# Kernel optimization log

Hardware: AMD Instinct MI355X
Metric: run time of the kernel (lower is better)

The kernel has to match this reference:

```python
import jax, jax.numpy as jnp
import numpy as np

D_MODEL = 768
NHEAD = 12
HEAD_DIM = D_MODEL // NHEAD


def setup_inputs() -> dict:
    key = jax.random.key(0)
    ks = jax.random.split(key, 9)
    B, S = 1, 4096
    scale = 1.0 / np.sqrt(D_MODEL)
    x = jax.random.normal(ks[0], (B, S, D_MODEL), dtype=jnp.float32)
    # Linear params: weight [out,in] torch convention, bias [out]
    wq = jax.random.normal(ks[1], (D_MODEL, D_MODEL), dtype=jnp.float32) * scale
    bq = jnp.zeros((D_MODEL,), dtype=jnp.float32)
    wk = jax.random.normal(ks[2], (D_MODEL, D_MODEL), dtype=jnp.float32) * scale
    bk = jnp.zeros((D_MODEL,), dtype=jnp.float32)
    wv = jax.random.normal(ks[3], (D_MODEL, D_MODEL), dtype=jnp.float32) * scale
    bv = jnp.zeros((D_MODEL,), dtype=jnp.float32)
    wo = jax.random.normal(ks[4], (D_MODEL, D_MODEL), dtype=jnp.float32) * scale
    bo = jnp.zeros((D_MODEL,), dtype=jnp.float32)
    return {"x": x, "wq": wq, "bq": bq, "wk": wk, "bk": bk,
            "wv": wv, "bv": bv, "wo": wo, "bo": bo}


def reference(x, wq, bq, wk, bk, wv, bv, wo, bo):
    B, S, D = x.shape
    H, Hd = NHEAD, HEAD_DIM
    # projections (torch Linear: x @ W^T + b)
    q = (x @ wq.T + bq).reshape(B, S, H, Hd).transpose(0, 2, 1, 3)  # [B,H,S,Hd]
    k = (x @ wk.T + bk).reshape(B, S, H, Hd).transpose(0, 2, 1, 3)
    v = (x @ wv.T + bv).reshape(B, S, H, Hd).transpose(0, 2, 1, 3)
    scores = jnp.einsum('bhsd,bhtd->bhst', q, k) / jnp.sqrt(jnp.float32(Hd))  # [B,H,S,S]
    probs = jax.nn.softmax(scores, axis=-1)
    attn = jnp.einsum('bhst,bhtd->bhsd', probs, v)  # [B,H,S,Hd]
    attn = attn.transpose(0, 2, 1, 3).reshape(B, S, D)
    return attn @ wo.T + bo
```

## Files before the change

### kernel.cpp

```cpp
#include <hip/hip_runtime.h>
#include <hip/hip_bf16.h>

typedef __attribute__((ext_vector_type(8))) __bf16 bf16x8;
typedef __attribute__((ext_vector_type(4))) __bf16 bf16x4;
typedef __attribute__((ext_vector_type(4))) float f32x4;

#define D_MODEL 768
#define SEQ     4096
#define NH      12
#define HD      64

#define QSCALE (0.125f * 1.44269504088896f)

__device__ __forceinline__ void gload_lds16(const void* g, void* l) {
    __builtin_amdgcn_global_load_lds(
        (const __attribute__((address_space(1))) void*)g,
        (__attribute__((address_space(3))) void*)l, 16, 0, 0);
}

__global__ __launch_bounds__(256) void cvt_kernel(
    const float* __restrict__ x,  const float* __restrict__ wq,
    const float* __restrict__ wk, const float* __restrict__ wv,
    const float* __restrict__ wo,
    __bf16* __restrict__ xb,  __bf16* __restrict__ wqb,
    __bf16* __restrict__ wkb, __bf16* __restrict__ wvb,
    __bf16* __restrict__ wob)
{
    const int XV = SEQ * D_MODEL / 4;
    const int WV = D_MODEL * D_MODEL / 4;
    const int total = XV + 4 * WV;
    for (int i = blockIdx.x * blockDim.x + threadIdx.x; i < total;
         i += gridDim.x * blockDim.x) {
        const float* src; __bf16* dst; int j;
        if      (i < XV)          { src = x;  dst = xb;  j = i; }
        else if (i < XV + WV)     { src = wq; dst = wqb; j = i - XV; }
        else if (i < XV + 2*WV)   { src = wk; dst = wkb; j = i - XV - WV; }
        else if (i < XV + 3*WV)   { src = wv; dst = wvb; j = i - XV - 2*WV; }
        else                      { src = wo; dst = wob; j = i - XV - 3*WV; }
        float4 v = ((const float4*)src)[j];
        bf16x4 o;
        o[0] = (__bf16)v.x; o[1] = (__bf16)v.y;
        o[2] = (__bf16)v.z; o[3] = (__bf16)v.w;
        ((bf16x4*)dst)[j] = o;
    }
}

__device__ __forceinline__ void gemm128_core(
    const __bf16* __restrict__ A, const __bf16* __restrict__ B, int KD,
    f32x4 acc[4][4], __bf16 (*As)[64], __bf16 (*Bs)[64])
{
    const int t = threadIdx.x;
    const int lane = t & 63, wid = t >> 6;
    const int wm = (wid & 1) * 64, wn = (wid >> 1) * 64;
    const int lr = lane & 15, lc = lane >> 4;
    const int rl = lane >> 3;
    const int cs = (lane & 7) ^ rl;

    const __bf16* ag = A + (size_t)(wid * 32 + rl) * KD + cs * 8;
    const __bf16* bg = B + (size_t)(wid * 32 + rl) * KD + cs * 8;

    for (int kt = 0; kt < KD / 64; ++kt) {
        __syncthreads();
        #pragma unroll
        for (int i = 0; i < 4; ++i) {
            gload_lds16(ag + (size_t)i * 8 * KD + kt * 64,
                        &As[wid * 32 + i * 8][0]);
            gload_lds16(bg + (size_t)i * 8 * KD + kt * 64,
                        &Bs[wid * 32 + i * 8][0]);
        }
        __syncthreads();

        #pragma unroll
        for (int kh = 0; kh < 2; ++kh) {
            bf16x8 af[4], bfr[4];
            #pragma unroll
            for (int mi = 0; mi < 4; ++mi)
                af[mi] = *(const bf16x8*)
                    &As[wm + mi * 16 + lr][(((kh << 2) | lc) ^ (lr & 7)) * 8];
            #pragma unroll
            for (int ni = 0; ni < 4; ++ni)
                bfr[ni] = *(const bf16x8*)
                    &Bs[wn + ni * 16 + lr][(((kh << 2) | lc) ^ (lr & 7)) * 8];
            __builtin_amdgcn_s_setprio(1);
            #pragma unroll
            for (int mi = 0; mi < 4; ++mi)
                #pragma unroll
                for (int ni = 0; ni < 4; ++ni)
                    acc[mi][ni] = __builtin_amdgcn_mfma_f32_16x16x32_bf16(
                        af[mi], bfr[ni], acc[mi][ni], 0, 0, 0);
            __builtin_amdgcn_s_setprio(0);
        }
    }
}

__global__ __launch_bounds__(256) void qkv_gemm(
    const __bf16* __restrict__ xb,
    const __bf16* __restrict__ wqb, const __bf16* __restrict__ wkb,
    const __bf16* __restrict__ wvb,
    const float* __restrict__ bq, const float* __restrict__ bk,
    const float* __restrict__ bv,
    __bf16* __restrict__ Qo, __bf16* __restrict__ Ko,
    __bf16* __restrict__ Vto)
{
    __shared__ __bf16 As[128][64];
    __shared__ __bf16 Bs[128][64];
    const int bm = blockIdx.x;
    const int seg = blockIdx.y / 6, bn = blockIdx.y % 6;
    const __bf16* B  = (seg == 0) ? wqb : (seg == 1) ? wkb : wvb;
    const float* bias = (seg == 0) ? bq : (seg == 1) ? bk : bv;

    f32x4 acc[4][4] = {};
    gemm128_core(xb + (size_t)bm * 128 * D_MODEL,
                 B  + (size_t)bn * 128 * D_MODEL, D_MODEL, acc, As, Bs);

    const int t = threadIdx.x, lane = t & 63, wid = t >> 6;
    const int wm = (wid & 1) * 64, wn = (wid >> 1) * 64;
    const int lr = lane & 15, lc = lane >> 4;
    const int m0 = bm * 128 + wm, n0 = bn * 128 + wn;

    if (seg < 2) {
        __bf16* O = (seg == 0) ? Qo : Ko;
        const float sc = (seg == 0) ? QSCALE : 1.0f;
        #pragma unroll
        for (int mi = 0; mi < 4; ++mi)
            #pragma unroll
            for (int ni = 0; ni < 4; ++ni) {
                int col = n0 + ni * 16 + lr;
                float bb = bias[col];
                #pragma unroll
                for (int r = 0; r < 4; ++r)
                    O[(size_t)(m0 + mi * 16 + lc * 4 + r) * D_MODEL + col] =
                        (__bf16)((acc[mi][ni][r] + bb) * sc);
            }
    } else {
        #pragma unroll
        for (int mi = 0; mi < 4; ++mi)
            #pragma unroll
            for (int ni = 0; ni < 4; ++ni) {
                int col = n0 + ni * 16 + lr;
                float bb = bias[col];
                bf16x4 pk;
                #pragma unroll
                for (int r = 0; r < 4; ++r)
                    pk[r] = (__bf16)(acc[mi][ni][r] + bb);
                *(bf16x4*)&Vto[(size_t)col * SEQ + m0 + mi * 16 + lc * 4] = pk;
            }
    }
}

__global__ __launch_bounds__(256) void attn_kernel(
    const __bf16* __restrict__ Q, const __bf16* __restrict__ K,
    const __bf16* __restrict__ Vt, __bf16* __restrict__ Attn)
{
    __shared__ __bf16 Ks[2][64][64];
    __shared__ __bf16 Vs[2][64][64];
    __shared__ __bf16 Ps[4][16][64];

    const int bid = blockIdx.x;
    const int swz = (bid & 7) * 96 + (bid >> 3);
    const int h  = swz >> 6;
    const int q0 = (swz & 63) * 64;

    const int t = threadIdx.x, lane = t & 63, wid = t >> 6;
    const int lr = lane & 15, lc = lane >> 4;
    const int rl = lane >> 3;
    const int cs = (lane & 7) ^ rl;
    const int sx = lr & 7;

    const __bf16* kg = K  + (size_t)(wid * 16 + rl) * D_MODEL + h * HD + cs * 8;
    const __bf16* vg = Vt + (size_t)(h * HD + wid * 16 + rl) * SEQ + cs * 8;

    const __bf16* qrow = Q + (size_t)(q0 + wid * 16 + lr) * D_MODEL + h * HD;
    bf16x8 qf0 = *(const bf16x8*)&qrow[lc * 8];
    bf16x8 qf1 = *(const bf16x8*)&qrow[32 + lc * 8];

    f32x4 acc[4] = {};
    float m_r = -1e30f, l_r = 0.f;

    {
        gload_lds16(kg,                 &Ks[0][wid * 16 + 0][0]);
        gload_lds16(kg + 8 * D_MODEL,   &Ks[0][wid * 16 + 8][0]);
        gload_lds16(vg,                 &Vs[0][wid * 16 + 0][0]);
        gload_lds16(vg + 8 * SEQ,       &Vs[0][wid * 16 + 8][0]);
    }

    const int NT = SEQ / 64;
    for (int kt = 0; kt < NT; ++kt) {
        const int cur = kt & 1;
        __syncthreads();

        if (kt + 1 < NT) {
            const int nxt = cur ^ 1;
            const size_t ko = (size_t)(kt + 1) * 64 * D_MODEL;
            const size_t vo = (size_t)(kt + 1) * 64;
            gload_lds16(kg + ko,               &Ks[nxt][wid * 16 + 0][0]);
            gload_lds16(kg + ko + 8 * D_MODEL, &Ks[nxt][wid * 16 + 8][0]);
            gload_lds16(vg + vo,               &Vs[nxt][wid * 16 + 0][0]);
            gload_lds16(vg + vo + 8 * SEQ,     &Vs[nxt][wid * 16 + 8][0]);
        }

        bf16x8 kf[4][2];
        #pragma unroll
        for (int nt = 0; nt < 4; ++nt) {
            kf[nt][0] = *(const bf16x8*)&Ks[cur][nt * 16 + lr][(lc ^ sx) * 8];
            kf[nt][1] = *(const bf16x8*)&Ks[cur][nt * 16 + lr][((4 | lc) ^ sx) * 8];
        }
        f32x4 st[4];
        __builtin_amdgcn_s_setprio(1);
        #pragma unroll
        for (int nt = 0; nt < 4; ++nt) {
            f32x4 s = {};
            s = __builtin_amdgcn_mfma_f32_16x16x32_bf16(kf[nt][0], qf0, s, 0, 0, 0);
            s = __builtin_amdgcn_mfma_f32_16x16x32_bf16(kf[nt][1], qf1, s, 0, 0, 0);
            st[nt] = s;
        }
        __builtin_amdgcn_s_setprio(0);

        float mx = -1e30f;
        #pragma unroll
        for (int nt = 0; nt < 4; ++nt)
            #pragma unroll
            for (int r = 0; r < 4; ++r)
                mx = fmaxf(mx, st[nt][r]);
        mx = fmaxf(mx, __shfl_xor(mx, 16, 64));
        mx = fmaxf(mx, __shfl_xor(mx, 32, 64));

        const bool skip = (bool)__all(mx - m_r <= 8.0f);
        float mnew = skip ? m_r : fmaxf(m_r, mx);
        float corr = skip ? 1.0f : exp2f(m_r - mnew);

        float rs = 0.f;
        float pv[4][4];
        #pragma unroll
        for (int nt = 0; nt < 4; ++nt)
            #pragma unroll
            for (int r = 0; r < 4; ++r) {
                float p = exp2f(st[nt][r] - mnew);
                pv[nt][r] = p;
                rs += p;
            }
        rs += __shfl_xor(rs, 16, 64);
        rs += __shfl_xor(rs, 32, 64);
        l_r = l_r * corr + rs;
        m_r = mnew;

        if (!skip) {
            #pragma unroll
            for (int r = 0; r < 4; ++r) {
                float cq = __shfl(corr, lc * 4 + r, 64);
                #pragma unroll
                for (int dt = 0; dt < 4; ++dt)
                    acc[dt][r] *= cq;
            }
        }

        #pragma unroll
        for (int nt = 0; nt < 4; ++nt) {
            union { __bf16 hh[4]; uint2 u; } w;
            w.hh[0] = (__bf16)pv[nt][0]; w.hh[1] = (__bf16)pv[nt][1];
            w.hh[2] = (__bf16)pv[nt][2]; w.hh[3] = (__bf16)pv[nt][3];
            const int pb = (((nt << 1) | (lc >> 1)) ^ sx) * 8 + (lc & 1) * 4;
            *(uint2*)&Ps[wid][lr][pb] = w.u;
        }

        bf16x8 pa0 = *(const bf16x8*)&Ps[wid][lr][(lc ^ sx) * 8];
        bf16x8 pa1 = *(const bf16x8*)&Ps[wid][lr][((4 | lc) ^ sx) * 8];
        __builtin_amdgcn_s_setprio(1);
        #pragma unroll
        for (int dt = 0; dt < 4; ++dt) {
            bf16x8 vf0 = *(const bf16x8*)&Vs[cur][dt * 16 + lr][(lc ^ sx) * 8];
            bf16x8 vf1 = *(const bf16x8*)&Vs[cur][dt * 16 + lr][((4 | lc) ^ sx) * 8];
            acc[dt] = __builtin_amdgcn_mfma_f32_16x16x32_bf16(pa0, vf0, acc[dt], 0, 0, 0);
            acc[dt] = __builtin_amdgcn_mfma_f32_16x16x32_bf16(pa1, vf1, acc[dt], 0, 0, 0);
        }
        __builtin_amdgcn_s_setprio(0);
    }

    #pragma unroll
    for (int r = 0; r < 4; ++r) {
        float linv = 1.0f / __shfl(l_r, lc * 4 + r, 64);
        #pragma unroll
        for (int dt = 0; dt < 4; ++dt)
            Attn[(size_t)(q0 + wid * 16 + lc * 4 + r) * D_MODEL
                 + h * HD + dt * 16 + lr] = (__bf16)(acc[dt][r] * linv);
    }
}

__global__ __launch_bounds__(256) void out_gemm(
    const __bf16* __restrict__ Ab, const __bf16* __restrict__ wob,
    const float* __restrict__ bo, float* __restrict__ out)
{
    __shared__ __bf16 As[128][64];
    __shared__ __bf16 Bs[128][64];
    const int bm = blockIdx.x, bn = blockIdx.y;
    f32x4 acc[4][4] = {};
    gemm128_core(Ab  + (size_t)bm * 128 * D_MODEL,
                 wob + (size_t)bn * 128 * D_MODEL, D_MODEL, acc, As, Bs);

    const int t = threadIdx.x, lane = t & 63, wid = t >> 6;
    const int wm = (wid & 1) * 64, wn = (wid >> 1) * 64;
    const int lr = lane & 15, lc = lane >> 4;
    const int m0 = bm * 128 + wm, n0 = bn * 128 + wn;
    #pragma unroll
    for (int mi = 0; mi < 4; ++mi)
        #pragma unroll
        for (int ni = 0; ni < 4; ++ni) {
            int col = n0 + ni * 16 + lr;
            float bb = bo[col];
            #pragma unroll
            for (int r = 0; r < 4; ++r)
                out[(size_t)(m0 + mi * 16 + lc * 4 + r) * D_MODEL + col] =
                    acc[mi][ni][r] + bb;
        }
}

extern "C" void kernel_launch(void* const* d_in, const int* in_sizes, int n_in,
                              void* d_out, int out_size, void* d_ws, size_t ws_size,
                              hipStream_t stream) {
    const float* x  = (const float*)d_in[0];
    const float* wq = (const float*)d_in[1];
    const float* bq = (const float*)d_in[2];
    const float* wk = (const float*)d_in[3];
    const float* bk = (const float*)d_in[4];
    const float* wv = (const float*)d_in[5];
    const float* bv = (const float*)d_in[6];
    const float* wo = (const float*)d_in[7];
    const float* bo = (const float*)d_in[8];

    char* ws = (char*)d_ws;
    const size_t XB_SZ = (size_t)SEQ * D_MODEL * 2;
    const size_t W_SZ  = (size_t)D_MODEL * D_MODEL * 2;
    __bf16* xb  = (__bf16*)(ws);
    __bf16* wqb = (__bf16*)(ws + XB_SZ);
    __bf16* wkb = (__bf16*)(ws + XB_SZ + W_SZ);
    __bf16* wvb = (__bf16*)(ws + XB_SZ + 2 * W_SZ);
    __bf16* wob = (__bf16*)(ws + XB_SZ + 3 * W_SZ);
    __bf16* Qb  = (__bf16*)(ws + XB_SZ + 4 * W_SZ);
    __bf16* Kb  = (__bf16*)(ws + 2 * XB_SZ + 4 * W_SZ);
    __bf16* Vtb = (__bf16*)(ws + 3 * XB_SZ + 4 * W_SZ);
    __bf16* Ab  = (__bf16*)(ws + 4 * XB_SZ + 4 * W_SZ);

    cvt_kernel<<<1024, 256, 0, stream>>>(x, wq, wk, wv, wo,
                                         xb, wqb, wkb, wvb, wob);
    qkv_gemm<<<dim3(32, 18), 256, 0, stream>>>(xb, wqb, wkb, wvb,
                                               bq, bk, bv, Qb, Kb, Vtb);
    attn_kernel<<<768, 256, 0, stream>>>(Qb, Kb, Vtb, Ab);
    out_gemm<<<dim3(32, 6), 256, 0, stream>>>(Ab, wob, bo, (float*)d_out);
}
```

Before: 180.9 us.

## Use 32x32x16 MFMA in attention with 2 waves of 32 query rows

Restructures the attention kernel so each block runs 2 waves instead of 4, with each wave handling 32 query rows through 32x32x16 bf16 MFMAs instead of 16x16x32. The 32-row layout puts one query row per lane, so row max, row sum and rescaling need only a single cross-half shuffle, and output stores are vectorized. Each K/V tile is still shared per block but loaded by fewer threads, and higher register use per wave may limit occupancy.

```diff
diff --git a/kernel.cpp b/kernel.cpp
--- a/kernel.cpp
+++ b/kernel.cpp
@@ -4,6 +4,7 @@
 typedef __attribute__((ext_vector_type(8))) __bf16 bf16x8;
 typedef __attribute__((ext_vector_type(4))) __bf16 bf16x4;
 typedef __attribute__((ext_vector_type(4))) float f32x4;
+typedef __attribute__((ext_vector_type(16))) float f32x16;
 
 #define D_MODEL 768
 #define SEQ     4096
@@ -148,13 +149,13 @@
     }
 }
 
-__global__ __launch_bounds__(256) void attn_kernel(
+__global__ __launch_bounds__(128) void attn_kernel(
     const __bf16* __restrict__ Q, const __bf16* __restrict__ K,
     const __bf16* __restrict__ Vt, __bf16* __restrict__ Attn)
 {
     __shared__ __bf16 Ks[2][64][64];
     __shared__ __bf16 Vs[2][64][64];
-    __shared__ __bf16 Ps[4][16][64];
+    __shared__ __bf16 Ps[2][32][64];
 
     const int bid = blockIdx.x;
     const int swz = (bid & 7) * 96 + (bid >> 3);
@@ -162,27 +163,36 @@
     const int q0 = (swz & 63) * 64;
 
     const int t = threadIdx.x, lane = t & 63, wid = t >> 6;
-    const int lr = lane & 15, lc = lane >> 4;
+    const int ql = lane & 31;
+    const int hi = lane >> 5;
     const int rl = lane >> 3;
     const int cs = (lane & 7) ^ rl;
-    const int sx = lr & 7;
-
-    const __bf16* kg = K  + (size_t)(wid * 16 + rl) * D_MODEL + h * HD + cs * 8;
-    const __bf16* vg = Vt + (size_t)(h * HD + wid * 16 + rl) * SEQ + cs * 8;
-
-    const __bf16* qrow = Q + (size_t)(q0 + wid * 16 + lr) * D_MODEL + h * HD;
-    bf16x8 qf0 = *(const bf16x8*)&qrow[lc * 8];
-    bf16x8 qf1 = *(const bf16x8*)&qrow[32 + lc * 8];
-
-    f32x4 acc[4] = {};
+    const int sx = lane & 7;
+
+    const __bf16* kg = K  + (size_t)(wid * 32 + rl) * D_MODEL + h * HD + cs * 8;
+    const __bf16* vg = Vt + (size_t)(h * HD + wid * 32 + rl) * SEQ + cs * 8;
+
+    const __bf16* qrow = Q + (size_t)(q0 + wid * 32 + ql) * D_MODEL + h * HD;
+    bf16x8 qf[4];
+    #pragma unroll
+    for (int k4 = 0; k4 < 4; ++k4)
+        qf[k4] = *(const bf16x8*)&qrow[k4 * 16 + hi * 8];
+
+    f32x16 acc0 = {}, acc1 = {};
     float m_r = -1e30f, l_r = 0.f;
 
-    {
-        gload_lds16(kg,                 &Ks[0][wid * 16 + 0][0]);
-        gload_lds16(kg + 8 * D_MODEL,   &Ks[0][wid * 16 + 8][0]);
-        gload_lds16(vg,                 &Vs[0][wid * 16 + 0][0]);
-        gload_lds16(vg + 8 * SEQ,       &Vs[0][wid * 16 + 8][0]);
-    }
+    #pragma unroll
+    for (int i = 0; i < 4; ++i) {
+        gload_lds16(kg + (size_t)i * 8 * D_MODEL, &Ks[0][wid * 32 + i * 8][0]);
+        gload_lds16(vg + (size_t)i * 8 * SEQ,     &Vs[0][wid * 32 + i * 8][0]);
+    }
+
+    #define PWRITE(kvb, v0, v1) do {                                         \
+        union { __bf16 h2[2]; unsigned u; } t_;                              \
+        t_.h2[0] = (__bf16)(v0); t_.h2[1] = (__bf16)(v1);                    \
+        *(unsigned*)&Ps[wid][ql][((((kvb) >> 3) ^ sx) << 3) + ((kvb) & 7)]   \
+            = t_.u;                                                          \
+    } while (0)
 
     const int NT = SEQ / 64;
     for (int kt = 0; kt < NT; ++kt) {
@@ -191,38 +201,36 @@
 
         if (kt + 1 < NT) {
             const int nxt = cur ^ 1;
-            const size_t ko = (size_t)(kt + 1) * 64 * D_MODEL;
-            const size_t vo = (size_t)(kt + 1) * 64;
-            gload_lds16(kg + ko,               &Ks[nxt][wid * 16 + 0][0]);
-            gload_lds16(kg + ko + 8 * D_MODEL, &Ks[nxt][wid * 16 + 8][0]);
-            gload_lds16(vg + vo,               &Vs[nxt][wid * 16 + 0][0]);
-            gload_lds16(vg + vo + 8 * SEQ,     &Vs[nxt][wid * 16 + 8][0]);
-        }
-
-        bf16x8 kf[4][2];
-        #pragma unroll
-        for (int nt = 0; nt < 4; ++nt) {
-            kf[nt][0] = *(const bf16x8*)&Ks[cur][nt * 16 + lr][(lc ^ sx) * 8];
-            kf[nt][1] = *(const bf16x8*)&Ks[cur][nt * 16 + lr][((4 | lc) ^ sx) * 8];
-        }
-        f32x4 st[4];
+            const __bf16* kgt = kg + (size_t)(kt + 1) * 64 * D_MODEL;
+            const __bf16* vgt = vg + (size_t)(kt + 1) * 64;
+            #pragma unroll
+            for (int i = 0; i < 4; ++i) {
+                gload_lds16(kgt + (size_t)i * 8 * D_MODEL,
+                            &Ks[nxt][wid * 32 + i * 8][0]);
+                gload_lds16(vgt + (size_t)i * 8 * SEQ,
+                            &Vs[nxt][wid * 32 + i * 8][0]);
+            }
+        }
+
+        f32x16 st0 = {}, st1 = {};
         __builtin_amdgcn_s_setprio(1);
         #pragma unroll
-        for (int nt = 0; nt < 4; ++nt) {
-            f32x4 s = {};
-            s = __builtin_amdgcn_mfma_f32_16x16x32_bf16(kf[nt][0], qf0, s, 0, 0, 0);
-            s = __builtin_amdgcn_mfma_f32_16x16x32_bf16(kf[nt][1], qf1, s, 0, 0, 0);
-            st[nt] = s;
+        for (int k4 = 0; k4 < 4; ++k4) {
+            bf16x8 kf0 = *(const bf16x8*)
+                &Ks[cur][ql][((k4 * 2 + hi) ^ sx) * 8];
+            bf16x8 kf1 = *(const bf16x8*)
+                &Ks[cur][32 + ql][((k4 * 2 + hi) ^ sx) * 8];
+            st0 = __builtin_amdgcn_mfma_f32_32x32x16_bf16(kf0, qf[k4], st0, 0, 0, 0);
+            st1 = __builtin_amdgcn_mfma_f32_32x32x16_bf16(kf1, qf[k4], st1, 0, 0, 0);
         }
         __builtin_amdgcn_s_setprio(0);
 
         float mx = -1e30f;
         #pragma unroll
-        for (int nt = 0; nt < 4; ++nt)
-            #pragma unroll
-            for (int r = 0; r < 4; ++r)
-                mx = fmaxf(mx, st[nt][r]);
-        mx = fmaxf(mx, __shfl_xor(mx, 16, 64));
+        for (int r = 0; r < 16; ++r) {
+            mx = fmaxf(mx, st0[r]);
+            mx = fmaxf(mx, st1[r]);
+        }
         mx = fmaxf(mx, __shfl_xor(mx, 32, 64));
 
         const bool skip = (bool)__all(mx - m_r <= 8.0f);
@@ -230,59 +238,60 @@
         float corr = skip ? 1.0f : exp2f(m_r - mnew);
 
         float rs = 0.f;
-        float pv[4][4];
-        #pragma unroll
-        for (int nt = 0; nt < 4; ++nt)
-            #pragma unroll
-            for (int r = 0; r < 4; ++r) {
-                float p = exp2f(st[nt][r] - mnew);
-                pv[nt][r] = p;
-                rs += p;
-            }
-        rs += __shfl_xor(rs, 16, 64);
+        #pragma unroll
+        for (int r = 0; r < 16; ++r) {
+            st0[r] = exp2f(st0[r] - mnew);
+            st1[r] = exp2f(st1[r] - mnew);
+            rs += st0[r] + st1[r];
+        }
         rs += __shfl_xor(rs, 32, 64);
         l_r = l_r * corr + rs;
         m_r = mnew;
 
         if (!skip) {
             #pragma unroll
-            for (int r = 0; r < 4; ++r) {
-                float cq = __shfl(corr, lc * 4 + r, 64);
-                #pragma unroll
-                for (int dt = 0; dt < 4; ++dt)
-                    acc[dt][r] *= cq;
-            }
-        }
-
-        #pragma unroll
-        for (int nt = 0; nt < 4; ++nt) {
-            union { __bf16 hh[4]; uint2 u; } w;
-            w.hh[0] = (__bf16)pv[nt][0]; w.hh[1] = (__bf16)pv[nt][1];
-            w.hh[2] = (__bf16)pv[nt][2]; w.hh[3] = (__bf16)pv[nt][3];
-            const int pb = (((nt << 1) | (lc >> 1)) ^ sx) * 8 + (lc & 1) * 4;
-            *(uint2*)&Ps[wid][lr][pb] = w.u;
-        }
-
-        bf16x8 pa0 = *(const bf16x8*)&Ps[wid][lr][(lc ^ sx) * 8];
-        bf16x8 pa1 = *(const bf16x8*)&Ps[wid][lr][((4 | lc) ^ sx) * 8];
+            for (int r = 0; r < 16; ++r) { acc0[r] *= corr; acc1[r] *= corr; }
+        }
+
+        #pragma unroll
+        for (int qd = 0; qd < 4; ++qd) {
+            PWRITE(8 * qd + 4 * hi,          st0[4 * qd + 0], st0[4 * qd + 1]);
+            PWRITE(8 * qd + 4 * hi + 2,      st0[4 * qd + 2], st0[4 * qd + 3]);
+            PWRITE(32 + 8 * qd + 4 * hi,     st1[4 * qd + 0], st1[4 * qd + 1]);
+            PWRITE(32 + 8 * qd + 4 * hi + 2, st1[4 * qd + 2], st1[4 * qd + 3]);
+        }
+
         __builtin_amdgcn_s_setprio(1);
         #pragma unroll
-        for (int dt = 0; dt < 4; ++dt) {
-            bf16x8 vf0 = *(const bf16x8*)&Vs[cur][dt * 16 + lr][(lc ^ sx) * 8];
-            bf16x8 vf1 = *(const bf16x8*)&Vs[cur][dt * 16 + lr][((4 | lc) ^ sx) * 8];
-            acc[dt] = __builtin_amdgcn_mfma_f32_16x16x32_bf16(pa0, vf0, acc[dt], 0, 0, 0);
-            acc[dt] = __builtin_amdgcn_mfma_f32_16x16x32_bf16(pa1, vf1, acc[dt], 0, 0, 0);
+        for (int kp = 0; kp < 4; ++kp) {
+            bf16x8 pf = *(const bf16x8*)
+                &Ps[wid][ql][((kp * 2 + hi) ^ sx) * 8];
+            bf16x8 vf0 = *(const bf16x8*)
+                &Vs[cur][ql][((kp * 2 + hi) ^ sx) * 8];
+            bf16x8 vf1 = *(const bf16x8*)
+                &Vs[cur][32 + ql][((kp * 2 + hi) ^ sx) * 8];
+            acc0 = __builtin_amdgcn_mfma_f32_32x32x16_bf16(vf0, pf, acc0, 0, 0, 0);
+            acc1 = __builtin_amdgcn_mfma_f32_32x32x16_bf16(vf1, pf, acc1, 0, 0, 0);
         }
         __builtin_amdgcn_s_setprio(0);
     }
-
+    #undef PWRITE
+
+    float linv = 1.0f / l_r;
+    __bf16* orow = Attn + (size_t)(q0 + wid * 32 + ql) * D_MODEL + h * HD + hi * 4;
     #pragma unroll
-    for (int r = 0; r < 4; ++r) {
-        float linv = 1.0f / __shfl(l_r, lc * 4 + r, 64);
-        #pragma unroll
-        for (int dt = 0; dt < 4; ++dt)
-            Attn[(size_t)(q0 + wid * 16 + lc * 4 + r) * D_MODEL
-                 + h * HD + dt * 16 + lr] = (__bf16)(acc[dt][r] * linv);
+    for (int g = 0; g < 4; ++g) {
+        union { __bf16 h4[4]; uint2 v2; } w;
+        w.h4[0] = (__bf16)(acc0[g * 4 + 0] * linv);
+        w.h4[1] = (__bf16)(acc0[g * 4 + 1] * linv);
+        w.h4[2] = (__bf16)(acc0[g * 4 + 2] * linv);
+        w.h4[3] = (__bf16)(acc0[g * 4 + 3] * linv);
+        *(uint2*)&orow[g * 8] = w.v2;
+        w.h4[0] = (__bf16)(acc1[g * 4 + 0] * linv);
+        w.h4[1] = (__bf16)(acc1[g * 4 + 1] * linv);
+        w.h4[2] = (__bf16)(acc1[g * 4 + 2] * linv);
+        w.h4[3] = (__bf16)(acc1[g * 4 + 3] * linv);
+        *(uint2*)&orow[32 + g * 8] = w.v2;
     }
 }
 
@@ -344,6 +353,6 @@
                                          xb, wqb, wkb, wvb, wob);
     qkv_gemm<<<dim3(32, 18), 256, 0, stream>>>(xb, wqb, wkb, wvb,
                                                bq, bk, bv, Qb, Kb, Vtb);
-    attn_kernel<<<768, 256, 0, stream>>>(Qb, Kb, Vtb, Ab);
+    attn_kernel<<<768, 128, 0, stream>>>(Qb, Kb, Vtb, Ab);
     out_gemm<<<dim3(32, 6), 256, 0, stream>>>(Ab, wob, bo, (float*)d_out);
 }
```

New measurement: 194.7 us. +7.6%, slower.
